# Kernel tuning notes

Measured on AMD Instinct MI355X. Metric: run time of the kernel, lower is better.

Reference implementation:

```python
import jax, jax.numpy as jnp
import numpy as np

B, T, D, H, NB, K, CDIM, CTX = 8, 4096, 3, 128, 6, 20, 128, 7


def setup_inputs() -> dict:
    key = jax.random.key(0)
    ks = jax.random.split(key, 16)
    s = 0.05
    inp = {
        'p': jax.random.normal(ks[0], (B, T, D), jnp.float32),
        'W_pos': jax.random.normal(ks[1], (D, H), jnp.float32) * s,
        'b_pos': jnp.zeros((H,), jnp.float32),
        # ResnetBlockFC(2H -> H): fc_0(2H,H), fc_1(H,H), shortcut(2H,H, no bias)
        'blk_W0': jax.random.normal(ks[2], (NB, 2 * H, H), jnp.float32) * s,
        'blk_b0': jnp.zeros((NB, H), jnp.float32),
        'blk_W1': jax.random.normal(ks[3], (NB, H, H), jnp.float32) * s,
        'blk_b1': jnp.zeros((NB, H), jnp.float32),
        'blk_Ws': jax.random.normal(ks[4], (NB, 2 * H, H), jnp.float32) * s,
        # Attention: score MLP on context (dim 7 -> 1), output proj (H -> H)
        'att_Wc': jax.random.normal(ks[5], (NB, CTX, 1), jnp.float32) * s,
        'att_bc': jnp.zeros((NB, 1), jnp.float32),
        'att_Wo': jax.random.normal(ks[6], (NB, H, H), jnp.float32) * s,
        'att_bo': jnp.zeros((NB, H), jnp.float32),
        'W_c': jax.random.normal(ks[7], (H, CDIM), jnp.float32) * s,
        'b_c': jnp.zeros((CDIM,), jnp.float32),
    }
    return inp


def _knn(p):
    # squared pairwise distances [B,T,T], top-K smallest
    sq = jnp.sum(p * p, axis=-1)  # [B,T]
    d2 = sq[:, :, None] + sq[:, None, :] - 2.0 * jnp.einsum('btd,bsd->bts', p, p)
    neg, idx = jax.lax.top_k(-d2, K)            # idx: [B,T,K]
    dis = jnp.sqrt(jnp.maximum(-neg, 1e-12))    # euclidean distance [B,T,K]
    return dis, idx


def _gather(c, idx):
    # c: [B,T,h], idx: [B,T,K] -> [B,T,K,h]  (vectorized pool_local)
    return jax.vmap(lambda ci, ii: ci[ii])(c, idx)


def _resnet_block(x, W0, b0, W1, b1, Ws):
    # occupancy-networks ResnetBlockFC: shortcut(x) + fc_1(relu(fc_0(relu(x))))
    h = jnp.maximum(x, 0.0) @ W0 + b0
    dx = jnp.maximum(h, 0.0) @ W1 + b1
    return x @ Ws + dx


def reference(p, W_pos, b_pos, blk_W0, blk_b0, blk_W1, blk_b1, blk_Ws,
              att_Wc, att_bc, att_Wo, att_bo, W_c, b_c):
    dis, idx = _knn(p)
    pooled_points = _gather(p, idx)                                   # [B,T,K,3]
    p_rep = jnp.broadcast_to(p[:, :, None, :], (B, T, K, D))
    context = jnp.concatenate([dis[..., None], pooled_points, p_rep], axis=-1)  # [B,T,K,7]

    net = p @ W_pos + b_pos                                           # [B,T,H]
    last_net = jnp.zeros_like(net)
    for i in range(NB):
        pooled = _gather(net, idx)                                    # [B,T,K,H]
        # attention over the K neighbors, weights from context
        scores = context @ att_Wc[i] + att_bc[i]                      # [B,T,K,1]
        w = jax.nn.softmax(scores, axis=2)
        att = jnp.sum(w * pooled, axis=2) @ att_Wo[i] + att_bo[i]     # [B,T,H]
        x = jnp.concatenate([net, att], axis=2)                       # [B,T,2H]
        net = _resnet_block(x, blk_W0[i], blk_b0[i], blk_W1[i], blk_b1[i], blk_Ws[i])
        net = net + last_net
        last_net = net
    return net @ W_c + b_c                                            # [B,T,c_dim]
```

## Files before the change

kernel.cpp:

```cpp
#include <hip/hip_runtime.h>
#include <hip/hip_bf16.h>
#include <math.h>

#define BB 8
#define TT 4096
#define HHD 128
#define NBK 6
#define KNN 20
#define BT (BB*TT)

typedef __attribute__((ext_vector_type(8))) short bf16x8;
typedef __attribute__((ext_vector_type(4))) float f32x4;

__device__ __forceinline__ float b2f(unsigned short u){
  return __uint_as_float(((unsigned int)u) << 16);
}
__device__ __forceinline__ unsigned short f2b(float f){
  unsigned int x = __float_as_uint(f);
  unsigned int r = (x + 0x7fffu + ((x >> 16) & 1u)) >> 16;
  return (unsigned short)r;
}
__device__ __forceinline__ float ldp(const void* base, int i, int f32m){
  return f32m ? ((const float*)base)[i] : b2f(((const unsigned short*)base)[i]);
}
__device__ __forceinline__ float lo2f(unsigned int u){ return __uint_as_float(u << 16); }
__device__ __forceinline__ float hi2f(unsigned int u){ return __uint_as_float(u & 0xffff0000u); }
__device__ __forceinline__ unsigned int relu2(unsigned int u){
  unsigned int s = u & 0x80008000u;
  unsigned int m = s | (s - (s >> 15));
  return u & ~m;
}
__device__ __forceinline__ bf16x8 relu8(bf16x8 x){
  union { bf16x8 v; unsigned int u[4]; } t; t.v = x;
  t.u[0] = relu2(t.u[0]); t.u[1] = relu2(t.u[1]);
  t.u[2] = relu2(t.u[2]); t.u[3] = relu2(t.u[3]);
  return t.v;
}
__device__ __forceinline__ unsigned int splitpk(float v){
  unsigned short h = f2b(v);
  float hv = b2f(h);
  unsigned short l = f2b(v - hv);
  return (unsigned int)h | ((unsigned int)l << 16);
}

__global__ void k_detect(const unsigned short* __restrict__ wpos_raw, int* __restrict__ flag){
  int lane = threadIdx.x;
  int cnt = 0;
  for (int i = lane; i < 384; i += 64) {
    unsigned int e = (wpos_raw[i] >> 7) & 0xFFu;
    if (e >= 0x90u) cnt++;
  }
  #pragma unroll
  for (int off = 32; off > 0; off >>= 1) cnt += __shfl_down(cnt, off);
  if (lane == 0) *flag = (cnt > 10) ? 1 : 0;
}

__global__ __launch_bounds__(256) void k_prep_points(const void* __restrict__ p,
                                                     const int* __restrict__ flagp,
                                                     float4* __restrict__ pf4){
  int r = blockIdx.x*256 + threadIdx.x;
  if (r >= BT) return;
  int f32m = *flagp;
  float x = ldp(p, r*3+0, f32m), y = ldp(p, r*3+1, f32m), z = ldp(p, r*3+2, f32m);
  float sq = __fadd_rn(__fadd_rn(__fmul_rn(x,x), __fmul_rn(y,y)), __fmul_rn(z,z));
  pf4[r] = make_float4(x, y, z, sq);
}

__global__ __launch_bounds__(256) void k_net0(const float4* __restrict__ pf4,
                                              const void* __restrict__ Wpos,
                                              const void* __restrict__ bpos,
                                              const int* __restrict__ flagp,
                                              unsigned short* __restrict__ netA){
  int t = blockIdx.x*256 + threadIdx.x;
  int f32m = *flagp;
  int c = t & 127, r = t >> 7;
  float4 q = pf4[r];
  float v = ldp(bpos, c, f32m);
  v = fmaf(q.x, ldp(Wpos, c,       f32m), v);
  v = fmaf(q.y, ldp(Wpos, 128 + c, f32m), v);
  v = fmaf(q.z, ldp(Wpos, 256 + c, f32m), v);
  netA[t] = f2b(v);
}

__global__ __launch_bounds__(256) void k_transpose(const void* __restrict__ W0,
                                                   const void* __restrict__ W1,
                                                   const void* __restrict__ Ws,
                                                   const void* __restrict__ Wo,
                                                   const void* __restrict__ Wc,
                                                   const int* __restrict__ flagp,
                                                   unsigned short* __restrict__ wT){
  int t = blockIdx.x*256 + threadIdx.x;
  int f32m = *flagp;
  if (t < 196608) {
    int i = t >> 15; int rem = t & 32767; int n = rem >> 8; int k = rem & 255;
    wT[t] = f2b(ldp(W0, i*32768 + k*128 + n, f32m));
  } else if (t < 294912) {
    int u = t - 196608; int i = u >> 14; int rem = u & 16383; int n = rem >> 7; int k = rem & 127;
    wT[t] = f2b(ldp(W1, i*16384 + k*128 + n, f32m));
  } else if (t < 491520) {
    int u = t - 294912; int i = u >> 15; int rem = u & 32767; int n = rem >> 8; int k = rem & 255;
    wT[t] = f2b(ldp(Ws, i*32768 + k*128 + n, f32m));
  } else if (t < 589824) {
    int u = t - 491520; int i = u >> 14; int rem = u & 16383; int n = rem >> 7; int k = rem & 127;
    wT[t] = f2b(ldp(Wo, i*16384 + k*128 + n, f32m));
  } else if (t < 606208) {
    int u = t - 589824; int n = u >> 7; int k = u & 127;
    wT[t] = f2b(ldp(Wc, k*128 + n, f32m));
  }
}

#define INS(act, dv, iv) do { bool A_ = (act); float D_ = (dv); int I_ = (iv);        \
  _Pragma("unroll")                                                                    \
  for (int j = 19; j >= 1; --j) {                                                      \
    bool cj = A_ && (D_ < ld[j]); bool cm = A_ && (D_ < ld[j-1]);                      \
    ld[j] = cj ? (cm ? ld[j-1] : D_) : ld[j];                                          \
    li[j] = cj ? (cm ? li[j-1] : I_) : li[j];                                          \
  }                                                                                    \
  { bool c0 = A_ && (D_ < ld[0]); ld[0] = c0 ? D_ : ld[0]; li[0] = c0 ? I_ : li[0]; } \
} while(0)

#define KCAP   20
#define MARGIN 0.02f

#define KNN_FLUSH() do {                                                               \
  int mc_ = cnt;                                                                       \
  _Pragma("unroll")                                                                    \
  for (int o_ = 32; o_ > 0; o_ >>= 1) { int t_ = __shfl_xor(mc_, o_); mc_ = mc_ > t_ ? mc_ : t_; } \
  _Pragma("unroll 1")                                                                  \
  for (int u_ = 0; u_ < mc_; ++u_) {                                                   \
    float2 e_ = stk[u_*256 + tid];                                                     \
    bool act_ = u_ < cnt;                                                              \
    int piv_ = __float_as_int(e_.y);                                                   \
    float4 pp_ = tilef4[act_ ? (piv_ - ch*512) : 0];                                   \
    float dot_ = __fadd_rn(__fadd_rn(__fmul_rn(q.x,pp_.x), __fmul_rn(q.y,pp_.y)),      \
                           __fmul_rn(q.z,pp_.z));                                      \
    float d2e_ = __fsub_rn(__fadd_rn(q.w, pp_.w), __fmul_rn(2.0f, dot_));              \
    INS(act_, d2e_, piv_);                                                             \
  }                                                                                    \
  cnt = 0;                                                                             \
  atomicMin(&sthr[qlocal], __float_as_uint(fmaxf(ld[19], 0.0f)));                      \
  threshP = fminf(ld[19], __uint_as_float(sthr[qlocal])) + MARGIN;                     \
} while(0)

__global__ __launch_bounds__(256) void k_knn(const float4* __restrict__ pf4,
                                             const void* __restrict__ Wc,
                                             const void* __restrict__ bc,
                                             const int* __restrict__ flagp,
                                             unsigned short* __restrict__ idx16,
                                             unsigned short* __restrict__ wsoftb){
  __shared__ __align__(16) char smem[57344];
  __shared__ unsigned int sthr[64];
  float4* tilef4 = (float4*)smem;
  uint4*  tilesp = (uint4*)(smem + 8192);
  float2* stk    = (float2*)(smem + 16384);
  float*  lsd    = (float*)(smem + 16384);
  int*    lsi    = (int*)(smem + 36864);

  int tid  = threadIdx.x;
  int wv   = tid >> 6, lane = tid & 63;
  int cq   = lane & 15;
  int kg   = lane >> 4;
  int qlocal = wv*16 + cq;
  int b    = blockIdx.x >> 6;
  int f32m = *flagp;
  float4 q = pf4[blockIdx.x*64 + qlocal];

  if (tid < 64) sthr[tid] = 0x7F7FFFFFu;

  union FRU { bf16x8 v; unsigned int u[4]; };
  FRU bfr;
  {
    float e = (kg == 0) ? -2.0f*q.x : -2.0f*q.z;
    unsigned int ehl = splitpk(e);
    unsigned int eh = ehl & 0xffffu, el = ehl >> 16;
    float f = (kg == 0) ? -2.0f*q.y : q.w;
    unsigned int fhl = splitpk(f);
    unsigned int fh = fhl & 0xffffu, fl = fhl >> 16;
    unsigned int v0 = eh | (eh << 16);
    unsigned int v1 = el | (el << 16);
    unsigned int v2 = (kg == 0) ? (fh | (fh << 16)) : 0x3F803F80u;
    unsigned int v3 = (kg == 0) ? (fl | (fl << 16)) : fhl;
    if (kg >= 2) { v0 = 0; v1 = 0; v2 = 0; v3 = 0; }
    bfr.u[0] = v0; bfr.u[1] = v1; bfr.u[2] = v2; bfr.u[3] = v3;
  }
  const f32x4 zf = {0.f, 0.f, 0.f, 0.f};

  float ld[20]; int li[20];
  #pragma unroll
  for (int j = 0; j < 20; ++j) { ld[j] = 3.0e38f; li[j] = 0; }
  float threshP = 3.0e38f;
  int cnt = 0;

  for (int ch = 0; ch < 8; ++ch) {
    __syncthreads();
    {
      const float4* src = pf4 + (b << 12) + ch*512;
      float4 a0 = src[tid], a1 = src[tid + 256];
      tilef4[tid]       = a0;
      tilef4[tid + 256] = a1;
      tilesp[tid]       = make_uint4(splitpk(a0.x), splitpk(a0.y), splitpk(a0.z), splitpk(a0.w));
      tilesp[tid + 256] = make_uint4(splitpk(a1.x), splitpk(a1.y), splitpk(a1.z), splitpk(a1.w));
    }
    __syncthreads();
    threshP = fminf(ld[19], __uint_as_float(sthr[qlocal])) + MARGIN;
    #pragma unroll 4
    for (int g = 0; g < 32; ++g) {
      uint4 s = tilesp[g*16 + cq];
      unsigned int u0 = (kg == 0) ? s.x : s.z;
      unsigned int u2 = (kg == 0) ? s.y : s.w;
      unsigned int u3 = (kg == 0) ? u2 : 0x3F803F80u;
      if (kg >= 2) { u0 = 0; u2 = 0; u3 = 0; }
      FRU afr; afr.u[0] = u0; afr.u[1] = u0; afr.u[2] = u2; afr.u[3] = u3;
      f32x4 dd = __builtin_amdgcn_mfma_f32_16x16x32_bf16(afr.v, bfr.v, zf, 0, 0, 0);
      int pbase = ch*512 + g*16 + kg*4;
      #pragma unroll
      for (int r = 0; r < 4; ++r) {
        if (dd[r] < threshP) {
          stk[cnt*256 + tid] = make_float2(dd[r], __int_as_float(pbase + r));
          cnt++;
        }
      }
      if (__ballot(cnt >= KCAP-3)) KNN_FLUSH();
    }
    if (__ballot(cnt > 0)) KNN_FLUSH();
  }

  __syncthreads();
  #pragma unroll
  for (int j = 0; j < 20; ++j) { lsd[tid*20 + j] = ld[j]; lsi[tid*20 + j] = li[j]; }
  __syncthreads();

  if (tid < 64) {
    int w2 = tid >> 4, c2 = tid & 15;
    int base = w2*64 + c2;
    int p0 = base*20, p1 = (base+16)*20, p2 = (base+32)*20, p3 = (base+48)*20;
    int i0 = 0, i1 = 0, i2 = 0, i3 = 0;
    int rq = blockIdx.x*64 + tid;
    float4 qq = pf4[rq];
    float dis[20]; int outi[20];
    #pragma unroll
    for (int o = 0; o < 20; ++o) {
      float d0 = lsd[p0+i0], d1 = lsd[p1+i1], d2v = lsd[p2+i2], d3 = lsd[p3+i3];
      int   j0 = lsi[p0+i0], j1 = lsi[p1+i1], j2  = lsi[p2+i2], j3 = lsi[p3+i3];
      float bd = d0; int bi = j0; int sel = 0;
      if (d1  < bd || (d1  == bd && j1 < bi)) { bd = d1;  bi = j1; sel = 1; }
      if (d2v < bd || (d2v == bd && j2 < bi)) { bd = d2v; bi = j2; sel = 2; }
      if (d3  < bd || (d3  == bd && j3 < bi)) { bd = d3;  bi = j3; sel = 3; }
      i0 += (sel==0); i1 += (sel==1); i2 += (sel==2); i3 += (sel==3);
      dis[o] = sqrtf(fmaxf(bd, 1e-12f));
      outi[o] = bi;
    }
    float nx[20], ny[20], nz[20];
    #pragma unroll
    for (int k = 0; k < 20; ++k) {
      idx16[rq*20 + k] = (unsigned short)outi[k];
      float4 pp = pf4[(b << 12) + outi[k]];
      nx[k] = pp.x; ny[k] = pp.y; nz[k] = pp.z;
    }
    for (int i = 0; i < NBK; ++i) {
      float w0 = ldp(Wc,i*7+0,f32m), w1 = ldp(Wc,i*7+1,f32m), w2 = ldp(Wc,i*7+2,f32m);
      float w3 = ldp(Wc,i*7+3,f32m), w4 = ldp(Wc,i*7+4,f32m), w5 = ldp(Wc,i*7+5,f32m);
      float w6 = ldp(Wc,i*7+6,f32m);
      float bci = ldp(bc,i,f32m);
      float s[20]; float mx = -3.0e38f;
      #pragma unroll
      for (int k = 0; k < 20; ++k) {
        float v = bci;
        v = fmaf(dis[k], w0, v);
        v = fmaf(nx[k], w1, v); v = fmaf(ny[k], w2, v); v = fmaf(nz[k], w3, v);
        v = fmaf(qq.x, w4, v);  v = fmaf(qq.y, w5, v);  v = fmaf(qq.z, w6, v);
        s[k] = v; mx = fmaxf(mx, v);
      }
      float sum = 0.f;
      #pragma unroll
      for (int k = 0; k < 20; ++k) { float e = __expf(s[k] - mx); s[k] = e; sum += e; }
      float inv = 1.0f / sum;
      #pragma unroll
      for (int k = 0; k < 20; ++k) wsoftb[(rq*6 + i)*20 + k] = f2b(s[k]*inv);
    }
  }
}

__global__ __launch_bounds__(128) void k_block(const unsigned short* __restrict__ netIn,
                                               unsigned short* __restrict__ netOut,
                                               const unsigned short* __restrict__ idx16,
                                               const unsigned short* __restrict__ wsoftb,
                                               const unsigned short* __restrict__ wT,
                                               const void* __restrict__ b0s,
                                               const void* __restrict__ b1s,
                                               const void* __restrict__ bos,
                                               const int* __restrict__ flagp,
                                               int iblk, int hasResid){
  __shared__ unsigned short ldsA[16*136];
  __shared__ unsigned short ldsH[16*136];
  int tid = threadIdx.x;
  int f32m = *flagp;
  int c = tid >> 6, lane = tid & 63;
  int b  = blockIdx.x & 7;
  int r0 = (b << 12) + ((blockIdx.x >> 3) << 4);
  const unsigned short* W0T = wT + iblk*32768;
  const unsigned short* W1T = wT + 196608 + iblk*16384;
  const unsigned short* WsT = wT + 294912 + iblk*32768;
  const unsigned short* WoT = wT + 491520 + iblk*16384;
  int m = lane & 15, qd = lane >> 4;

  {
    int r = lane >> 2, cg = lane & 3;
    int grow = r0 + r;
    int cbase = c*64 + cg*16;
    const unsigned int* ip = (const unsigned int*)(idx16 + grow*20);
    const unsigned int* wp = (const unsigned int*)(wsoftb + (grow*6 + iblk)*20);
    const unsigned short* nbase = netIn + (b << 12)*128 + cbase;
    float acc[16];
    #pragma unroll
    for (int j = 0; j < 16; ++j) acc[j] = 0.f;
    #pragma unroll 2
    for (int kk = 0; kk < 10; ++kk) {
      unsigned int pair  = ip[kk];
      unsigned int wpair = wp[kk];
      int nb0 = (int)(pair & 4095u);
      int nb1 = (int)((pair >> 16) & 4095u);
      float wk0 = lo2f(wpair);
      float wk1 = hi2f(wpair);
      const uint4* np0 = (const uint4*)(nbase + nb0*128);
      const uint4* np1 = (const uint4*)(nbase + nb1*128);
      uint4 a0 = np0[0], b0_ = np0[1];
      uint4 a1 = np1[0], b1_ = np1[1];
      acc[0]  = fmaf(wk0, lo2f(a0.x),  acc[0]);
      acc[1]  = fmaf(wk0, hi2f(a0.x),  acc[1]);
      acc[2]  = fmaf(wk0, lo2f(a0.y),  acc[2]);
      acc[3]  = fmaf(wk0, hi2f(a0.y),  acc[3]);
      acc[4]  = fmaf(wk0, lo2f(a0.z),  acc[4]);
      acc[5]  = fmaf(wk0, hi2f(a0.z),  acc[5]);
      acc[6]  = fmaf(wk0, lo2f(a0.w),  acc[6]);
      acc[7]  = fmaf(wk0, hi2f(a0.w),  acc[7]);
      acc[8]  = fmaf(wk0, lo2f(b0_.x), acc[8]);
      acc[9]  = fmaf(wk0, hi2f(b0_.x), acc[9]);
      acc[10] = fmaf(wk0, lo2f(b0_.y), acc[10]);
      acc[11] = fmaf(wk0, hi2f(b0_.y), acc[11]);
      acc[12] = fmaf(wk0, lo2f(b0_.z), acc[12]);
      acc[13] = fmaf(wk0, hi2f(b0_.z), acc[13]);
      acc[14] = fmaf(wk0, lo2f(b0_.w), acc[14]);
      acc[15] = fmaf(wk0, hi2f(b0_.w), acc[15]);
      acc[0]  = fmaf(wk1, lo2f(a1.x),  acc[0]);
      acc[1]  = fmaf(wk1, hi2f(a1.x),  acc[1]);
      acc[2]  = fmaf(wk1, lo2f(a1.y),  acc[2]);
      acc[3]  = fmaf(wk1, hi2f(a1.y),  acc[3]);
      acc[4]  = fmaf(wk1, lo2f(a1.z),  acc[4]);
      acc[5]  = fmaf(wk1, hi2f(a1.z),  acc[5]);
      acc[6]  = fmaf(wk1, lo2f(a1.w),  acc[6]);
      acc[7]  = fmaf(wk1, hi2f(a1.w),  acc[7]);
      acc[8]  = fmaf(wk1, lo2f(b1_.x), acc[8]);
      acc[9]  = fmaf(wk1, hi2f(b1_.x), acc[9]);
      acc[10] = fmaf(wk1, lo2f(b1_.y), acc[10]);
      acc[11] = fmaf(wk1, hi2f(b1_.y), acc[11]);
      acc[12] = fmaf(wk1, lo2f(b1_.z), acc[12]);
      acc[13] = fmaf(wk1, hi2f(b1_.z), acc[13]);
      acc[14] = fmaf(wk1, lo2f(b1_.w), acc[14]);
      acc[15] = fmaf(wk1, hi2f(b1_.w), acc[15]);
    }
    #pragma unroll
    for (int j = 0; j < 8; ++j) {
      unsigned int pr = ((unsigned int)f2b(acc[2*j+1]) << 16) | (unsigned int)f2b(acc[2*j]);
      *(unsigned int*)(ldsH + r*136 + cbase + 2*j) = pr;
    }
  }
  __syncthreads();

  {
    bf16x8 asf[4];
    #pragma unroll
    for (int ks = 0; ks < 4; ++ks)
      asf[ks] = *(const bf16x8*)(ldsH + m*136 + ks*32 + qd*8);
    f32x4 acc2[4];
    #pragma unroll
    for (int i = 0; i < 4; ++i) { f32x4 z = {0.f,0.f,0.f,0.f}; acc2[i] = z; }
    #pragma unroll
    for (int i = 0; i < 4; ++i) {
      int cti = c*4 + i;
      const unsigned short* bp = WoT + (cti*16 + m)*128 + qd*8;
      #pragma unroll
      for (int ks = 0; ks < 4; ++ks)
        acc2[i] = __builtin_amdgcn_mfma_f32_16x16x32_bf16(asf[ks], *(const bf16x8*)(bp + ks*32), acc2[i], 0, 0, 0);
    }
    #pragma unroll
    for (int i = 0; i < 4; ++i) {
      int col = (c*4 + i)*16 + m;
      float bo = ldp(bos, iblk*128 + col, f32m);
      #pragma unroll
      for (int rr = 0; rr < 4; ++rr)
        ldsA[(qd*4 + rr)*136 + col] = f2b(acc2[i][rr] + bo);
    }
  }
  __syncthreads();

  bf16x8 nf[4], af[4];
  {
    const unsigned short* nrow = netIn + (r0 + m)*128;
    #pragma unroll
    for (int ks = 0; ks < 4; ++ks) nf[ks] = *(const bf16x8*)(nrow + ks*32 + qd*8);
    #pragma unroll
    for (int ks = 0; ks < 4; ++ks) af[ks] = *(const bf16x8*)(ldsA + m*136 + ks*32 + qd*8);
    bf16x8 rnf[4], raf[4];
    #pragma unroll
    for (int ks = 0; ks < 4; ++ks) { rnf[ks] = relu8(nf[ks]); raf[ks] = relu8(af[ks]); }
    f32x4 acc3[4];
    #pragma unroll
    for (int i = 0; i < 4; ++i) { f32x4 z = {0.f,0.f,0.f,0.f}; acc3[i] = z; }
    #pragma unroll
    for (int i = 0; i < 4; ++i) {
      int cti = c*4 + i;
      const unsigned short* bp = W0T + (cti*16 + m)*256 + qd*8;
      #pragma unroll
      for (int ks = 0; ks < 4; ++ks)
        acc3[i] = __builtin_amdgcn_mfma_f32_16x16x32_bf16(rnf[ks], *(const bf16x8*)(bp + ks*32), acc3[i], 0, 0, 0);
      #pragma unroll
      for (int ks = 0; ks < 4; ++ks)
        acc3[i] = __builtin_amdgcn_mfma_f32_16x16x32_bf16(raf[ks], *(const bf16x8*)(bp + 128 + ks*32), acc3[i], 0, 0, 0);
    }
    #pragma unroll
    for (int i = 0; i < 4; ++i) {
      int col = (c*4 + i)*16 + m;
      float b0v = ldp(b0s, iblk*128 + col, f32m);
      #pragma unroll
      for (int rr = 0; rr < 4; ++rr)
        ldsH[(qd*4 + rr)*136 + col] = f2b(fmaxf(acc3[i][rr] + b0v, 0.f));
    }
  }
  __syncthreads();

  {
    bf16x8 hf[4];
    #pragma unroll
    for (int ks = 0; ks < 4; ++ks) hf[ks] = *(const bf16x8*)(ldsH + m*136 + ks*32 + qd*8);
    f32x4 acc4[4];
    #pragma unroll
    for (int i = 0; i < 4; ++i) { f32x4 z = {0.f,0.f,0.f,0.f}; acc4[i] = z; }
    #pragma unroll
    for (int i = 0; i < 4; ++i) {
      int cti = c*4 + i;
      const unsigned short* bp1 = W1T + (cti*16 + m)*128 + qd*8;
      #pragma unroll
      for (int ks = 0; ks < 4; ++ks)
        acc4[i] = __builtin_amdgcn_mfma_f32_16x16x32_bf16(hf[ks], *(const bf16x8*)(bp1 + ks*32), acc4[i], 0, 0, 0);
      const unsigned short* bps = WsT + (cti*16 + m)*256 + qd*8;
      #pragma unroll
      for (int ks = 0; ks < 4; ++ks)
        acc4[i] = __builtin_amdgcn_mfma_f32_16x16x32_bf16(nf[ks], *(const bf16x8*)(bps + ks*32), acc4[i], 0, 0, 0);
      #pragma unroll
      for (int ks = 0; ks < 4; ++ks)
        acc4[i] = __builtin_amdgcn_mfma_f32_16x16x32_bf16(af[ks], *(const bf16x8*)(bps + 128 + ks*32), acc4[i], 0, 0, 0);
    }
    #pragma unroll
    for (int i = 0; i < 4; ++i) {
      int col = (c*4 + i)*16 + m;
      float b1v = ldp(b1s, iblk*128 + col, f32m);
      #pragma unroll
      for (int rr = 0; rr < 4; ++rr) {
        int grow2 = r0 + qd*4 + rr;
        float v = acc4[i][rr] + b1v;
        if (hasResid) v += b2f(netIn[grow2*128 + col]);
        netOut[grow2*128 + col] = f2b(v);
      }
    }
  }
}

__global__ __launch_bounds__(256) void k_final(const unsigned short* __restrict__ netIn,
                                               const unsigned short* __restrict__ WcT,
                                               const void* __restrict__ bcv,
                                               const int* __restrict__ flagp,
                                               void* __restrict__ out){
  int tid = threadIdx.x; int w = tid >> 6, lane = tid & 63;
  int f32m = *flagp;
  int t = w >> 1, c = w & 1;
  int r0 = blockIdx.x*32 + t*16;
  int m = lane & 15, qd = lane >> 4;
  bf16x8 nf[4];
  #pragma unroll
  for (int ks = 0; ks < 4; ++ks)
    nf[ks] = *(const bf16x8*)(netIn + (r0 + m)*128 + ks*32 + qd*8);
  f32x4 acc[4];
  #pragma unroll
  for (int i = 0; i < 4; ++i) { f32x4 z = {0.f,0.f,0.f,0.f}; acc[i] = z; }
  #pragma unroll
  for (int i = 0; i < 4; ++i) {
    int cti = c*4 + i;
    const unsigned short* bp = WcT + (cti*16 + m)*128 + qd*8;
    #pragma unroll
    for (int ks = 0; ks < 4; ++ks)
      acc[i] = __builtin_amdgcn_mfma_f32_16x16x32_bf16(nf[ks], *(const bf16x8*)(bp + ks*32), acc[i], 0, 0, 0);
  }
  if (f32m) {
    float* o = (float*)out;
    #pragma unroll
    for (int i = 0; i < 4; ++i) {
      int col = (c*4 + i)*16 + m;
      float bcf = ldp(bcv, col, 1);
      #pragma unroll
      for (int rr = 0; rr < 4; ++rr)
        o[(r0 + qd*4 + rr)*128 + col] = acc[i][rr] + bcf;
    }
  } else {
    unsigned short* o = (unsigned short*)out;
    #pragma unroll
    for (int i = 0; i < 4; ++i) {
      int col = (c*4 + i)*16 + m;
      float bcf = ldp(bcv, col, 0);
      #pragma unroll
      for (int rr = 0; rr < 4; ++rr)
        o[(r0 + qd*4 + rr)*128 + col] = f2b(acc[i][rr] + bcf);
    }
  }
}

extern "C" void kernel_launch(void* const* d_in, const int* in_sizes, int n_in,
                              void* d_out, int out_size, void* d_ws, size_t ws_size,
                              hipStream_t stream){
  const void* p    = d_in[0];
  const void* Wpos = d_in[1];
  const void* bpos = d_in[2];
  const void* W0   = d_in[3];
  const void* b0   = d_in[4];
  const void* W1   = d_in[5];
  const void* b1   = d_in[6];
  const void* Ws   = d_in[7];
  const void* Wc_  = d_in[8];
  const void* bc_  = d_in[9];
  const void* Wo   = d_in[10];
  const void* bo   = d_in[11];
  const void* WC   = d_in[12];
  const void* bC   = d_in[13];

  char* ws = (char*)d_ws;
  int*            flag   = (int*)(ws + 0);
  float4*         pf4    = (float4*)(ws + 256);
  unsigned short* idx16  = (unsigned short*)(ws + 524544);
  unsigned short* wsoftb = (unsigned short*)(ws + 1835264);
  unsigned short* netA   = (unsigned short*)(ws + 9699584);
  unsigned short* wT     = (unsigned short*)(ws + 18088192);

  k_detect     <<<dim3(1),     dim3(64),  0, stream>>>((const unsigned short*)Wpos, flag);
  k_prep_points<<<dim3(128),   dim3(256), 0, stream>>>(p, flag, pf4);
  k_net0       <<<dim3(16384), dim3(256), 0, stream>>>(pf4, Wpos, bpos, flag, netA);
  k_transpose  <<<dim3(2368),  dim3(256), 0, stream>>>(W0, W1, Ws, Wo, WC, flag, wT);
  k_knn        <<<dim3(512),   dim3(256), 0, stream>>>(pf4, Wc_, bc_, flag, idx16, wsoftb);

  unsigned short* a   = netA;
  unsigned short* bpt = (unsigned short*)d_out;
  for (int i = 0; i < 6; ++i) {
    k_block<<<dim3(2048), dim3(128), 0, stream>>>(a, bpt, idx16, wsoftb, wT,
                                                  b0, b1, bo, flag, i, (i > 0) ? 1 : 0);
    unsigned short* t = a; a = bpt; bpt = t;
  }
  k_final<<<dim3(1024), dim3(256), 0, stream>>>(a, wT + 589824, bC, flag, d_out);
}
```

Baseline: 616.3 us.

## Fuse six per-block launches into one persistent kernel with grid barriers

The six separate k_block launches become a single kernel that loops over the six blocks. Between stages it uses a global atomic counter barrier, which k_detect resets, with net buffers ping-ponging inside the kernel. This removes five kernel launches and their tails. In exchange it requires all 2048 workgroups to be co-resident, hinted by launch_bounds(128,4), or the spin barrier deadlocks, and it adds barrier spin and fence costs.

```diff
diff --git a/kernel.cpp b/kernel.cpp
--- a/kernel.cpp
+++ b/kernel.cpp
@@ -43,8 +43,10 @@
   return (unsigned int)h | ((unsigned int)l << 16);
 }
 
-__global__ void k_detect(const unsigned short* __restrict__ wpos_raw, int* __restrict__ flag){
+__global__ void k_detect(const unsigned short* __restrict__ wpos_raw, int* __restrict__ flag,
+                         unsigned int* __restrict__ bar){
   int lane = threadIdx.x;
+  if (lane < 8) bar[lane] = 0u;
   int cnt = 0;
   for (int i = lane; i < 384; i += 64) {
     unsigned int e = (wpos_raw[i] >> 7) & 0xFFu;
@@ -281,16 +283,16 @@
   }
 }
 
-__global__ __launch_bounds__(128) void k_block(const unsigned short* __restrict__ netIn,
-                                               unsigned short* __restrict__ netOut,
-                                               const unsigned short* __restrict__ idx16,
-                                               const unsigned short* __restrict__ wsoftb,
-                                               const unsigned short* __restrict__ wT,
-                                               const void* __restrict__ b0s,
-                                               const void* __restrict__ b1s,
-                                               const void* __restrict__ bos,
-                                               const int* __restrict__ flagp,
-                                               int iblk, int hasResid){
+__global__ __launch_bounds__(128, 4) void k_block6(unsigned short* __restrict__ netA,
+                                                   unsigned short* __restrict__ netB,
+                                                   const unsigned short* __restrict__ idx16,
+                                                   const unsigned short* __restrict__ wsoftb,
+                                                   const unsigned short* __restrict__ wT,
+                                                   const void* __restrict__ b0s,
+                                                   const void* __restrict__ b1s,
+                                                   const void* __restrict__ bos,
+                                                   const int* __restrict__ flagp,
+                                                   unsigned int* __restrict__ bar){
   __shared__ unsigned short ldsA[16*136];
   __shared__ unsigned short ldsH[16*136];
   int tid = threadIdx.x;
@@ -298,170 +300,190 @@
   int c = tid >> 6, lane = tid & 63;
   int b  = blockIdx.x & 7;
   int r0 = (b << 12) + ((blockIdx.x >> 3) << 4);
-  const unsigned short* W0T = wT + iblk*32768;
-  const unsigned short* W1T = wT + 196608 + iblk*16384;
-  const unsigned short* WsT = wT + 294912 + iblk*32768;
-  const unsigned short* WoT = wT + 491520 + iblk*16384;
   int m = lane & 15, qd = lane >> 4;
 
-  {
-    int r = lane >> 2, cg = lane & 3;
-    int grow = r0 + r;
-    int cbase = c*64 + cg*16;
-    const unsigned int* ip = (const unsigned int*)(idx16 + grow*20);
-    const unsigned int* wp = (const unsigned int*)(wsoftb + (grow*6 + iblk)*20);
-    const unsigned short* nbase = netIn + (b << 12)*128 + cbase;
-    float acc[16];
-    #pragma unroll
-    for (int j = 0; j < 16; ++j) acc[j] = 0.f;
-    #pragma unroll 2
-    for (int kk = 0; kk < 10; ++kk) {
-      unsigned int pair  = ip[kk];
-      unsigned int wpair = wp[kk];
-      int nb0 = (int)(pair & 4095u);
-      int nb1 = (int)((pair >> 16) & 4095u);
-      float wk0 = lo2f(wpair);
-      float wk1 = hi2f(wpair);
-      const uint4* np0 = (const uint4*)(nbase + nb0*128);
-      const uint4* np1 = (const uint4*)(nbase + nb1*128);
-      uint4 a0 = np0[0], b0_ = np0[1];
-      uint4 a1 = np1[0], b1_ = np1[1];
-      acc[0]  = fmaf(wk0, lo2f(a0.x),  acc[0]);
-      acc[1]  = fmaf(wk0, hi2f(a0.x),  acc[1]);
-      acc[2]  = fmaf(wk0, lo2f(a0.y),  acc[2]);
-      acc[3]  = fmaf(wk0, hi2f(a0.y),  acc[3]);
-      acc[4]  = fmaf(wk0, lo2f(a0.z),  acc[4]);
-      acc[5]  = fmaf(wk0, hi2f(a0.z),  acc[5]);
-      acc[6]  = fmaf(wk0, lo2f(a0.w),  acc[6]);
-      acc[7]  = fmaf(wk0, hi2f(a0.w),  acc[7]);
-      acc[8]  = fmaf(wk0, lo2f(b0_.x), acc[8]);
-      acc[9]  = fmaf(wk0, hi2f(b0_.x), acc[9]);
-      acc[10] = fmaf(wk0, lo2f(b0_.y), acc[10]);
-      acc[11] = fmaf(wk0, hi2f(b0_.y), acc[11]);
-      acc[12] = fmaf(wk0, lo2f(b0_.z), acc[12]);
-      acc[13] = fmaf(wk0, hi2f(b0_.z), acc[13]);
-      acc[14] = fmaf(wk0, lo2f(b0_.w), acc[14]);
-      acc[15] = fmaf(wk0, hi2f(b0_.w), acc[15]);
-      acc[0]  = fmaf(wk1, lo2f(a1.x),  acc[0]);
-      acc[1]  = fmaf(wk1, hi2f(a1.x),  acc[1]);
-      acc[2]  = fmaf(wk1, lo2f(a1.y),  acc[2]);
-      acc[3]  = fmaf(wk1, hi2f(a1.y),  acc[3]);
-      acc[4]  = fmaf(wk1, lo2f(a1.z),  acc[4]);
-      acc[5]  = fmaf(wk1, hi2f(a1.z),  acc[5]);
-      acc[6]  = fmaf(wk1, lo2f(a1.w),  acc[6]);
-      acc[7]  = fmaf(wk1, hi2f(a1.w),  acc[7]);
-      acc[8]  = fmaf(wk1, lo2f(b1_.x), acc[8]);
-      acc[9]  = fmaf(wk1, hi2f(b1_.x), acc[9]);
-      acc[10] = fmaf(wk1, lo2f(b1_.y), acc[10]);
-      acc[11] = fmaf(wk1, hi2f(b1_.y), acc[11]);
-      acc[12] = fmaf(wk1, lo2f(b1_.z), acc[12]);
-      acc[13] = fmaf(wk1, hi2f(b1_.z), acc[13]);
-      acc[14] = fmaf(wk1, lo2f(b1_.w), acc[14]);
-      acc[15] = fmaf(wk1, hi2f(b1_.w), acc[15]);
-    }
-    #pragma unroll
-    for (int j = 0; j < 8; ++j) {
-      unsigned int pr = ((unsigned int)f2b(acc[2*j+1]) << 16) | (unsigned int)f2b(acc[2*j]);
-      *(unsigned int*)(ldsH + r*136 + cbase + 2*j) = pr;
-    }
-  }
-  __syncthreads();
-
-  {
-    bf16x8 asf[4];
-    #pragma unroll
-    for (int ks = 0; ks < 4; ++ks)
-      asf[ks] = *(const bf16x8*)(ldsH + m*136 + ks*32 + qd*8);
-    f32x4 acc2[4];
-    #pragma unroll
-    for (int i = 0; i < 4; ++i) { f32x4 z = {0.f,0.f,0.f,0.f}; acc2[i] = z; }
-    #pragma unroll
-    for (int i = 0; i < 4; ++i) {
-      int cti = c*4 + i;
-      const unsigned short* bp = WoT + (cti*16 + m)*128 + qd*8;
+  #pragma unroll 1
+  for (int iblk = 0; iblk < 6; ++iblk) {
+    const unsigned short* netIn  = (iblk & 1) ? netB : netA;
+    unsigned short*       netOut = (iblk & 1) ? netA : netB;
+    int hasResid = (iblk > 0) ? 1 : 0;
+    const unsigned short* W0T = wT + iblk*32768;
+    const unsigned short* W1T = wT + 196608 + iblk*16384;
+    const unsigned short* WsT = wT + 294912 + iblk*32768;
+    const unsigned short* WoT = wT + 491520 + iblk*16384;
+
+    {
+      int r = lane >> 2, cg2 = lane & 3;
+      int grow = r0 + r;
+      int cbase = c*64 + cg2*16;
+      const unsigned int* ip = (const unsigned int*)(idx16 + grow*20);
+      const unsigned int* wp = (const unsigned int*)(wsoftb + (grow*6 + iblk)*20);
+      const unsigned short* nbase = netIn + (b << 12)*128 + cbase;
+      float acc[16];
+      #pragma unroll
+      for (int j = 0; j < 16; ++j) acc[j] = 0.f;
+      #pragma unroll 2
+      for (int kk = 0; kk < 10; ++kk) {
+        unsigned int pair  = ip[kk];
+        unsigned int wpair = wp[kk];
+        int nb0 = (int)(pair & 4095u);
+        int nb1 = (int)((pair >> 16) & 4095u);
+        float wk0 = lo2f(wpair);
+        float wk1 = hi2f(wpair);
+        const uint4* np0 = (const uint4*)(nbase + nb0*128);
+        const uint4* np1 = (const uint4*)(nbase + nb1*128);
+        uint4 a0 = np0[0], b0_ = np0[1];
+        uint4 a1 = np1[0], b1_ = np1[1];
+        acc[0]  = fmaf(wk0, lo2f(a0.x),  acc[0]);
+        acc[1]  = fmaf(wk0, hi2f(a0.x),  acc[1]);
+        acc[2]  = fmaf(wk0, lo2f(a0.y),  acc[2]);
+        acc[3]  = fmaf(wk0, hi2f(a0.y),  acc[3]);
+        acc[4]  = fmaf(wk0, lo2f(a0.z),  acc[4]);
+        acc[5]  = fmaf(wk0, hi2f(a0.z),  acc[5]);
+        acc[6]  = fmaf(wk0, lo2f(a0.w),  acc[6]);
+        acc[7]  = fmaf(wk0, hi2f(a0.w),  acc[7]);
+        acc[8]  = fmaf(wk0, lo2f(b0_.x), acc[8]);
+        acc[9]  = fmaf(wk0, hi2f(b0_.x), acc[9]);
+        acc[10] = fmaf(wk0, lo2f(b0_.y), acc[10]);
+        acc[11] = fmaf(wk0, hi2f(b0_.y), acc[11]);
+        acc[12] = fmaf(wk0, lo2f(b0_.z), acc[12]);
+        acc[13] = fmaf(wk0, hi2f(b0_.z), acc[13]);
+        acc[14] = fmaf(wk0, lo2f(b0_.w), acc[14]);
+        acc[15] = fmaf(wk0, hi2f(b0_.w), acc[15]);
+        acc[0]  = fmaf(wk1, lo2f(a1.x),  acc[0]);
+        acc[1]  = fmaf(wk1, hi2f(a1.x),  acc[1]);
+        acc[2]  = fmaf(wk1, lo2f(a1.y),  acc[2]);
+        acc[3]  = fmaf(wk1, hi2f(a1.y),  acc[3]);
+        acc[4]  = fmaf(wk1, lo2f(a1.z),  acc[4]);
+        acc[5]  = fmaf(wk1, hi2f(a1.z),  acc[5]);
+        acc[6]  = fmaf(wk1, lo2f(a1.w),  acc[6]);
+        acc[7]  = fmaf(wk1, hi2f(a1.w),  acc[7]);
+        acc[8]  = fmaf(wk1, lo2f(b1_.x), acc[8]);
+        acc[9]  = fmaf(wk1, hi2f(b1_.x), acc[9]);
+        acc[10] = fmaf(wk1, lo2f(b1_.y), acc[10]);
+        acc[11] = fmaf(wk1, hi2f(b1_.y), acc[11]);
+        acc[12] = fmaf(wk1, lo2f(b1_.z), acc[12]);
+        acc[13] = fmaf(wk1, hi2f(b1_.z), acc[13]);
+        acc[14] = fmaf(wk1, lo2f(b1_.w), acc[14]);
+        acc[15] = fmaf(wk1, hi2f(b1_.w), acc[15]);
+      }
+      #pragma unroll
+      for (int j = 0; j < 8; ++j) {
+        unsigned int pr = ((unsigned int)f2b(acc[2*j+1]) << 16) | (unsigned int)f2b(acc[2*j]);
+        *(unsigned int*)(ldsH + r*136 + cbase + 2*j) = pr;
+      }
+    }
+    __syncthreads();
+
+    {
+      bf16x8 asf[4];
       #pragma unroll
       for (int ks = 0; ks < 4; ++ks)
-        acc2[i] = __builtin_amdgcn_mfma_f32_16x16x32_bf16(asf[ks], *(const bf16x8*)(bp + ks*32), acc2[i], 0, 0, 0);
-    }
-    #pragma unroll
-    for (int i = 0; i < 4; ++i) {
-      int col = (c*4 + i)*16 + m;
-      float bo = ldp(bos, iblk*128 + col, f32m);
-      #pragma unroll
-      for (int rr = 0; rr < 4; ++rr)
-        ldsA[(qd*4 + rr)*136 + col] = f2b(acc2[i][rr] + bo);
-    }
-  }
-  __syncthreads();
-
-  bf16x8 nf[4], af[4];
-  {
-    const unsigned short* nrow = netIn + (r0 + m)*128;
-    #pragma unroll
-    for (int ks = 0; ks < 4; ++ks) nf[ks] = *(const bf16x8*)(nrow + ks*32 + qd*8);
-    #pragma unroll
-    for (int ks = 0; ks < 4; ++ks) af[ks] = *(const bf16x8*)(ldsA + m*136 + ks*32 + qd*8);
-    bf16x8 rnf[4], raf[4];
-    #pragma unroll
-    for (int ks = 0; ks < 4; ++ks) { rnf[ks] = relu8(nf[ks]); raf[ks] = relu8(af[ks]); }
-    f32x4 acc3[4];
-    #pragma unroll
-    for (int i = 0; i < 4; ++i) { f32x4 z = {0.f,0.f,0.f,0.f}; acc3[i] = z; }
-    #pragma unroll
-    for (int i = 0; i < 4; ++i) {
-      int cti = c*4 + i;
-      const unsigned short* bp = W0T + (cti*16 + m)*256 + qd*8;
-      #pragma unroll
-      for (int ks = 0; ks < 4; ++ks)
-        acc3[i] = __builtin_amdgcn_mfma_f32_16x16x32_bf16(rnf[ks], *(const bf16x8*)(bp + ks*32), acc3[i], 0, 0, 0);
-      #pragma unroll
-      for (int ks = 0; ks < 4; ++ks)
-        acc3[i] = __builtin_amdgcn_mfma_f32_16x16x32_bf16(raf[ks], *(const bf16x8*)(bp + 128 + ks*32), acc3[i], 0, 0, 0);
-    }
-    #pragma unroll
-    for (int i = 0; i < 4; ++i) {
-      int col = (c*4 + i)*16 + m;
-      float b0v = ldp(b0s, iblk*128 + col, f32m);
-      #pragma unroll
-      for (int rr = 0; rr < 4; ++rr)
-        ldsH[(qd*4 + rr)*136 + col] = f2b(fmaxf(acc3[i][rr] + b0v, 0.f));
-    }
-  }
-  __syncthreads();
-
-  {
-    bf16x8 hf[4];
-    #pragma unroll
-    for (int ks = 0; ks < 4; ++ks) hf[ks] = *(const bf16x8*)(ldsH + m*136 + ks*32 + qd*8);
-    f32x4 acc4[4];
-    #pragma unroll
-    for (int i = 0; i < 4; ++i) { f32x4 z = {0.f,0.f,0.f,0.f}; acc4[i] = z; }
-    #pragma unroll
-    for (int i = 0; i < 4; ++i) {
-      int cti = c*4 + i;
-      const unsigned short* bp1 = W1T + (cti*16 + m)*128 + qd*8;
-      #pragma unroll
-      for (int ks = 0; ks < 4; ++ks)
-        acc4[i] = __builtin_amdgcn_mfma_f32_16x16x32_bf16(hf[ks], *(const bf16x8*)(bp1 + ks*32), acc4[i], 0, 0, 0);
-      const unsigned short* bps = WsT + (cti*16 + m)*256 + qd*8;
-      #pragma unroll
-      for (int ks = 0; ks < 4; ++ks)
-        acc4[i] = __builtin_amdgcn_mfma_f32_16x16x32_bf16(nf[ks], *(const bf16x8*)(bps + ks*32), acc4[i], 0, 0, 0);
-      #pragma unroll
-      for (int ks = 0; ks < 4; ++ks)
-        acc4[i] = __builtin_amdgcn_mfma_f32_16x16x32_bf16(af[ks], *(const bf16x8*)(bps + 128 + ks*32), acc4[i], 0, 0, 0);
-    }
-    #pragma unroll
-    for (int i = 0; i < 4; ++i) {
-      int col = (c*4 + i)*16 + m;
-      float b1v = ldp(b1s, iblk*128 + col, f32m);
-      #pragma unroll
-      for (int rr = 0; rr < 4; ++rr) {
-        int grow2 = r0 + qd*4 + rr;
-        float v = acc4[i][rr] + b1v;
-        if (hasResid) v += b2f(netIn[grow2*128 + col]);
-        netOut[grow2*128 + col] = f2b(v);
-      }
+        asf[ks] = *(const bf16x8*)(ldsH + m*136 + ks*32 + qd*8);
+      f32x4 acc2[4];
+      #pragma unroll
+      for (int i = 0; i < 4; ++i) { f32x4 z = {0.f,0.f,0.f,0.f}; acc2[i] = z; }
+      #pragma unroll
+      for (int i = 0; i < 4; ++i) {
+        int cti = c*4 + i;
+        const unsigned short* bp = WoT + (cti*16 + m)*128 + qd*8;
+        #pragma unroll
+        for (int ks = 0; ks < 4; ++ks)
+          acc2[i] = __builtin_amdgcn_mfma_f32_16x16x32_bf16(asf[ks], *(const bf16x8*)(bp + ks*32), acc2[i], 0, 0, 0);
+      }
+      #pragma unroll
+      for (int i = 0; i < 4; ++i) {
+        int col = (c*4 + i)*16 + m;
+        float bo = ldp(bos, iblk*128 + col, f32m);
+        #pragma unroll
+        for (int rr = 0; rr < 4; ++rr)
+          ldsA[(qd*4 + rr)*136 + col] = f2b(acc2[i][rr] + bo);
+      }
+    }
+    __syncthreads();
+
+    bf16x8 nf[4], af[4];
+    {
+      const unsigned short* nrow = netIn + (r0 + m)*128;
+      #pragma unroll
+      for (int ks = 0; ks < 4; ++ks) nf[ks] = *(const bf16x8*)(nrow + ks*32 + qd*8);
+      #pragma unroll
+      for (int ks = 0; ks < 4; ++ks) af[ks] = *(const bf16x8*)(ldsA + m*136 + ks*32 + qd*8);
+      bf16x8 rnf[4], raf[4];
+      #pragma unroll
+      for (int ks = 0; ks < 4; ++ks) { rnf[ks] = relu8(nf[ks]); raf[ks] = relu8(af[ks]); }
+      f32x4 acc3[4];
+      #pragma unroll
+      for (int i = 0; i < 4; ++i) { f32x4 z = {0.f,0.f,0.f,0.f}; acc3[i] = z; }
+      #pragma unroll
+      for (int i = 0; i < 4; ++i) {
+        int cti = c*4 + i;
+        const unsigned short* bp = W0T + (cti*16 + m)*256 + qd*8;
+        #pragma unroll
+        for (int ks = 0; ks < 4; ++ks)
+          acc3[i] = __builtin_amdgcn_mfma_f32_16x16x32_bf16(rnf[ks], *(const bf16x8*)(bp + ks*32), acc3[i], 0, 0, 0);
+        #pragma unroll
+        for (int ks = 0; ks < 4; ++ks)
+          acc3[i] = __builtin_amdgcn_mfma_f32_16x16x32_bf16(raf[ks], *(const bf16x8*)(bp + 128 + ks*32), acc3[i], 0, 0, 0);
+      }
+      #pragma unroll
+      for (int i = 0; i < 4; ++i) {
+        int col = (c*4 + i)*16 + m;
+        float b0v = ldp(b0s, iblk*128 + col, f32m);
+        #pragma unroll
+        for (int rr = 0; rr < 4; ++rr)
+          ldsH[(qd*4 + rr)*136 + col] = f2b(fmaxf(acc3[i][rr] + b0v, 0.f));
+      }
+    }
+    __syncthreads();
+
+    {
+      bf16x8 hf[4];
+      #pragma unroll
+      for (int ks = 0; ks < 4; ++ks) hf[ks] = *(const bf16x8*)(ldsH + m*136 + ks*32 + qd*8);
+      f32x4 acc4[4];
+      #pragma unroll
+      for (int i = 0; i < 4; ++i) { f32x4 z = {0.f,0.f,0.f,0.f}; acc4[i] = z; }
+      #pragma unroll
+      for (int i = 0; i < 4; ++i) {
+        int cti = c*4 + i;
+        const unsigned short* bp1 = W1T + (cti*16 + m)*128 + qd*8;
+        #pragma unroll
+        for (int ks = 0; ks < 4; ++ks)
+          acc4[i] = __builtin_amdgcn_mfma_f32_16x16x32_bf16(hf[ks], *(const bf16x8*)(bp1 + ks*32), acc4[i], 0, 0, 0);
+        const unsigned short* bps = WsT + (cti*16 + m)*256 + qd*8;
+        #pragma unroll
+        for (int ks = 0; ks < 4; ++ks)
+          acc4[i] = __builtin_amdgcn_mfma_f32_16x16x32_bf16(nf[ks], *(const bf16x8*)(bps + ks*32), acc4[i], 0, 0, 0);
+        #pragma unroll
+        for (int ks = 0; ks < 4; ++ks)
+          acc4[i] = __builtin_amdgcn_mfma_f32_16x16x32_bf16(af[ks], *(const bf16x8*)(bps + 128 + ks*32), acc4[i], 0, 0, 0);
+      }
+      #pragma unroll
+      for (int i = 0; i < 4; ++i) {
+        int col = (c*4 + i)*16 + m;
+        float b1v = ldp(b1s, iblk*128 + col, f32m);
+        #pragma unroll
+        for (int rr = 0; rr < 4; ++rr) {
+          int grow2 = r0 + qd*4 + rr;
+          float v = acc4[i][rr] + b1v;
+          if (hasResid) v += b2f(netIn[grow2*128 + col]);
+          netOut[grow2*128 + col] = f2b(v);
+        }
+      }
+    }
+
+    if (iblk < 5) {
+      __syncthreads();
+      if (tid == 0) {
+        __threadfence();
+        __hip_atomic_fetch_add(&bar[iblk], 1u, __ATOMIC_ACQ_REL, __HIP_MEMORY_SCOPE_AGENT);
+        while (__hip_atomic_load(&bar[iblk], __ATOMIC_ACQUIRE, __HIP_MEMORY_SCOPE_AGENT) < 2048u) {
+          __builtin_amdgcn_s_sleep(8);
+        }
+        __threadfence();
+      }
+      __syncthreads();
     }
   }
 }
@@ -534,24 +556,23 @@
 
   char* ws = (char*)d_ws;
   int*            flag   = (int*)(ws + 0);
+  unsigned int*   bar    = (unsigned int*)(ws + 128);
   float4*         pf4    = (float4*)(ws + 256);
   unsigned short* idx16  = (unsigned short*)(ws + 524544);
   unsigned short* wsoftb = (unsigned short*)(ws + 1835264);
   unsigned short* netA   = (unsigned short*)(ws + 9699584);
   unsigned short* wT     = (unsigned short*)(ws + 18088192);
 
-  k_detect     <<<dim3(1),     dim3(64),  0, stream>>>((const unsigned short*)Wpos, flag);
+  k_detect     <<<dim3(1),     dim3(64),  0, stream>>>((const unsigned short*)Wpos, flag, bar);
   k_prep_points<<<dim3(128),   dim3(256), 0, stream>>>(p, flag, pf4);
   k_net0       <<<dim3(16384), dim3(256), 0, stream>>>(pf4, Wpos, bpos, flag, netA);
   k_transpose  <<<dim3(2368),  dim3(256), 0, stream>>>(W0, W1, Ws, Wo, WC, flag, wT);
   k_knn        <<<dim3(512),   dim3(256), 0, stream>>>(pf4, Wc_, bc_, flag, idx16, wsoftb);
 
-  unsigned short* a   = netA;
-  unsigned short* bpt = (unsigned short*)d_out;
-  for (int i = 0; i < 6; ++i) {
-    k_block<<<dim3(2048), dim3(128), 0, stream>>>(a, bpt, idx16, wsoftb, wT,
-                                                  b0, b1, bo, flag, i, (i > 0) ? 1 : 0);
-    unsigned short* t = a; a = bpt; bpt = t;
-  }
-  k_final<<<dim3(1024), dim3(256), 0, stream>>>(a, wT + 589824, bC, flag, d_out);
-}
+  {
+    unsigned short* netB = (unsigned short*)d_out;
+    k_block6<<<dim3(2048), dim3(128), 0, stream>>>(netA, netB, idx16, wsoftb, wT,
+                                                   b0, b1, bo, flag, bar);
+  }
+  k_final<<<dim3(1024), dim3(256), 0, stream>>>(netA, wT + 589824, bC, flag, d_out);
+}
```

After: 2.276 ms. 269% more time.
